# Performance work log

Measured on AMD Instinct MI355X. Metric: run time of the kernel, lower is better.

The kernel has to match this reference:

```python
import jax, jax.numpy as jnp
import numpy as np

STEP = 2  # neighbor window size (init arg `step`)


def _shift_sums(x, step):
    # sum over shifted-left (before) and shifted-right (after) neighbor states,
    # zero-padded at the boundaries, for shifts 1..step. x: [B, L, H]
    before = sum(jnp.pad(x[:, :-s, :], ((0, 0), (s, 0), (0, 0))) for s in range(1, step + 1))
    after = sum(jnp.pad(x[:, s:, :], ((0, 0), (0, s), (0, 0))) for s in range(1, step + 1))
    return before, after


def _slstm_forward(word_inputs, mask, num_layers, init_h, init_c, Wx, Wh, Wi, Wd, b, gWx, gWh, gb):
    B, L, D = word_inputs.shape
    H = Wx.shape[-1]
    fm = mask.astype(word_inputs.dtype)          # [B, L]
    seq_mask = fm[:, :, None]                    # [B, L, 1]
    mask_score = (fm * 1e25 - 1e25)[:, :, None]  # -inf-like for padded positions

    emb = word_inputs * seq_mask                 # embedding_hidden_state_pre
    h = (init_h * 0.1 - 0.05) * seq_mask         # uniform(-0.05, 0.05) init
    c = (init_c * 0.1 - 0.05) * seq_mask
    dh = jnp.mean(h, axis=1)                     # dummy-node hidden [B, H]
    dc = jnp.mean(c, axis=1)                     # dummy-node cell   [B, H]

    for _ in range(num_layers):
        comb = jnp.mean(h, axis=1)               # combined word hidden [B, H]
        dh_rep = jnp.broadcast_to(dh[:, None, :], (B, L, H))
        dc_rep = jnp.broadcast_to(dc[:, None, :], (B, L, H))

        # --- dummy (sentence) node update ---
        g_d = jax.nn.sigmoid(dh @ gWx[0] + comb @ gWh[0] + gb[0])              # [B, H]
        g_o = jax.nn.sigmoid(dh @ gWx[1] + comb @ gWh[1] + gb[1])              # [B, H]
        g_f = jax.nn.sigmoid(dh_rep @ gWx[2] + h @ gWh[2] + gb[2])             # [B, L, H]
        scores = jnp.concatenate([g_f + mask_score, g_d[:, None, :]], axis=1)  # [B, L+1, H]
        scores = jax.nn.softmax(scores, axis=1)
        dummy_c = jnp.sum(scores[:, :L, :] * c, axis=1) + scores[:, L, :] * dc
        dummy_h = g_o * jnp.tanh(dummy_c)

        # --- word node updates ---
        hb, ha = _shift_sums(h, STEP)
        cb, ca = _shift_sums(c, STEP)
        cat_h = jnp.concatenate([hb, ha], axis=-1)  # [B, L, 2H]

        # 7 gates stacked: f1, f2, f3, f4, i, o, u -> pre: [7, B, L, H]
        pre = (jnp.einsum('blh,ghk->gblk', h, Wx)
               + jnp.einsum('blh,ghk->gblk', cat_h, Wh)
               + jnp.einsum('bld,gdk->gblk', emb, Wi)
               + jnp.einsum('blh,ghk->gblk', dh_rep, Wd)
               + b[:, None, None, :])
        sig = jax.nn.sigmoid(pre[:6])
        f1, f2, f3, f4, i_g, o_g = sig[0], sig[1], sig[2], sig[3], sig[4], sig[5]
        u = jnp.tanh(pre[6])

        # normalize the five forget/input gates via softmax across gates
        five = jax.nn.softmax(jnp.stack([f1, f2, f3, f4, i_g], axis=0), axis=0)
        c_new = five[0] * cb + five[1] * ca + five[2] * c + five[3] * dc_rep + five[4] * u
        h_new = o_g * jnp.tanh(c_new)

        h = h_new * seq_mask
        c = c_new * seq_mask
        dh, dc = dummy_h, dummy_c

    return h


def setup_inputs() -> dict:
    key = jax.random.key(0)
    ks = jax.random.split(key, 12)
    B, L, D, H, G = 32, 1024, 256, 256, 7
    s = 0.1  # stddev of param init in the torch module
    return {
        'word_inputs': jax.random.normal(ks[0], (B, L, D), jnp.float32),
        'mask': jnp.ones((B, L), jnp.int32),
        'num_layers': 3,
        'init_h': jax.random.uniform(ks[1], (B, L, H), jnp.float32),
        'init_c': jax.random.uniform(ks[2], (B, L, H), jnp.float32),
        'Wx': jax.random.normal(ks[3], (G, H, H), jnp.float32) * s,
        'Wh': jax.random.normal(ks[4], (G, 2 * H, H), jnp.float32) * s,
        'Wi': jax.random.normal(ks[5], (G, D, H), jnp.float32) * s,
        'Wd': jax.random.normal(ks[6], (G, H, H), jnp.float32) * s,
        'b': jax.random.normal(ks[7], (G, H), jnp.float32) * s,
        'gWx': jax.random.normal(ks[8], (3, H, H), jnp.float32) * s,
        'gWh': jax.random.normal(ks[9], (3, H, H), jnp.float32) * s,
        'gb': jax.random.normal(ks[10], (3, H), jnp.float32) * s,
    }


def reference(word_inputs, mask, num_layers, init_h, init_c, Wx, Wh, Wi, Wd, b, gWx, gWh, gb):
    return _slstm_forward(word_inputs, mask, num_layers, init_h, init_c, Wx, Wh, Wi, Wd, b, gWx, gWh, gb)
```

## Files before the change

kernel.cpp:

```cpp
#include <hip/hip_runtime.h>
#include <hip/hip_bf16.h>
#include <math.h>

#define BB 32
#define LL 1024
#define DD 256
#define HH 256
#define NG 7
#define HW (HH*HH)
#define WhS (2*HH*HH)

typedef short bf16x8 __attribute__((ext_vector_type(8)));
typedef float f32x4  __attribute__((ext_vector_type(4)));
typedef unsigned short u16;
typedef unsigned int u32;

__device__ __forceinline__ float sigm(float x){ return 1.0f/(1.0f + expf(-x)); }
__device__ __forceinline__ float fsig(float x){ return __fdividef(1.0f, 1.0f + __expf(-x)); }
__device__ __forceinline__ float ftanh(float x){ return 1.0f - __fdividef(2.0f, 1.0f + __expf(2.0f*x)); }
__device__ __forceinline__ u16 f2b(float f){
  u32 u = __float_as_uint(f);
  return (u16)((u + 0x7fffu + ((u>>16)&1u)) >> 16);
}
__device__ __forceinline__ float b2f(u16 b){ return __uint_as_float(((u32)b)<<16); }
__device__ __forceinline__ float4 ld4(const float* p){ return *reinterpret_cast<const float4*>(p); }

__device__ __forceinline__ u32 packf2(float lo, float hi){
  float2 s; s.x = lo; s.y = hi;
  __hip_bfloat162 r = __float22bfloat162_rn(s);
  return *reinterpret_cast<u32*>(&r);
}
__device__ __forceinline__ u32 bfadd2(u32 a, u32 b){
  float lo = __uint_as_float(a << 16)        + __uint_as_float(b << 16);
  float hi = __uint_as_float(a & 0xffff0000u) + __uint_as_float(b & 0xffff0000u);
  return packf2(lo, hi);
}

__device__ __forceinline__ void gload16(const void* g, void* l){
  __builtin_amdgcn_global_load_lds(
    (const __attribute__((address_space(1))) unsigned int*)g,
    (__attribute__((address_space(3))) unsigned int*)l, 16, 0, 0);
}
__device__ __forceinline__ f32x4 mfma16(bf16x8 a, bf16x8 b, f32x4 c){
  return __builtin_amdgcn_mfma_f32_16x16x32_bf16(a, b, c, 0, 0, 0);
}

__global__ __launch_bounds__(256) void k_init(const float* __restrict__ ih, const float* __restrict__ ic,
    const int* __restrict__ mask, u16* __restrict__ h, float* __restrict__ c){
  size_t n = (size_t)BB*LL*HH;
  for (size_t idx = (size_t)blockIdx.x*256 + threadIdx.x; idx < n; idx += (size_t)gridDim.x*256){
    float fm = (float)mask[idx>>8];
    h[idx] = f2b((ih[idx]*0.1f - 0.05f)*fm);
    c[idx] = (ic[idx]*0.1f - 0.05f)*fm;
  }
}

__global__ __launch_bounds__(256) void k_mean1(const u16* __restrict__ h, const float* __restrict__ c,
    float* __restrict__ pmh, float* __restrict__ pmc){
  int b = blockIdx.x, ch = blockIdx.y, k = threadIdx.x;
  const u16* hp = h + ((size_t)b*LL + ch*64)*HH + k;
  const float* cp = c + ((size_t)b*LL + ch*64)*HH + k;
  float sh = 0.f, sc = 0.f;
  for (int l = 0; l < 64; ++l){ sh += b2f(hp[(size_t)l*HH]); sc += cp[(size_t)l*HH]; }
  pmh[(size_t)(b*16+ch)*HH + k] = sh;
  pmc[(size_t)(b*16+ch)*HH + k] = sc;
}
__global__ __launch_bounds__(256) void k_mean2(const float* __restrict__ pmh, const float* __restrict__ pmc,
    float* __restrict__ comb, float* __restrict__ combc){
  int b = blockIdx.x, k = threadIdx.x;
  float sh = 0.f, sc = 0.f;
  for (int ch = 0; ch < 16; ++ch){
    sh += pmh[(size_t)(b*16+ch)*HH + k];
    sc += pmc[(size_t)(b*16+ch)*HH + k];
  }
  comb[b*HH+k]  = sh*(1.0f/LL);
  combc[b*HH+k] = sc*(1.0f/LL);
}

__global__ __launch_bounds__(256) void k_small(const float* __restrict__ dh, const float* __restrict__ comb,
    const float* __restrict__ gWx, const float* __restrict__ gWh, const float* __restrict__ gb,
    const float* __restrict__ Wd, const float* __restrict__ bias,
    float* __restrict__ g_d, float* __restrict__ g_o, float* __restrict__ gx2f, float* __restrict__ wd){
  __shared__ float dsh[HH], csh[HH];
  int b = blockIdx.x, g = blockIdx.y, k = threadIdx.x;
  dsh[k] = dh[b*HH+k]; csh[k] = comb[b*HH+k];
  __syncthreads();
  if (g < NG){
    float aw = bias[g*HH+k];
    const float* W = Wd + (size_t)g*HW + k;
    for (int j = 0; j < HH; ++j) aw += dsh[j]*W[(size_t)j*HH];
    wd[(size_t)(g*BB + b)*HH + k] = aw;
  } else {
    float ad = gb[0*HH+k], ao = gb[1*HH+k], ax = gb[2*HH+k];
    for (int j = 0; j < HH; ++j){
      float dv = dsh[j], cv = csh[j];
      ad += dv*gWx[j*HH+k]      + cv*gWh[j*HH+k];
      ao += dv*gWx[HW + j*HH+k] + cv*gWh[HW + j*HH+k];
      ax += dv*gWx[2*HW + j*HH+k];
    }
    g_d[b*HH+k] = sigm(ad);
    g_o[b*HH+k] = sigm(ao);
    gx2f[b*HH+k] = ax;
  }
}

__global__ __launch_bounds__(256) void k_wpack(const float* __restrict__ Wx, const float* __restrict__ Wh,
    const float* __restrict__ Wi, u16* __restrict__ Bp){
  int idx = blockIdx.x*256 + threadIdx.x;
  int img = idx / 14336, e = idx % 14336;
  int nt = img >> 5, ks = img & 31;
  int g = e >> 11, r = e & 2047;
  int n = r >> 5, kblk = (r>>3)&3, j = r&7;
  int K = ks*32 + kblk*8 + j;
  int N = nt*64 + n;
  int slice = K >> 8, kr = K & 255;
  float v;
  if (slice == 0)      v = Wx[(size_t)g*HW  + (size_t)kr*HH + N];
  else if (slice == 1) v = Wh[(size_t)g*WhS + (size_t)kr*HH + N];
  else if (slice == 2) v = Wh[(size_t)g*WhS + (size_t)(256+kr)*HH + N];
  else                 v = Wi[(size_t)g*HW  + (size_t)kr*HH + N];
  Bp[idx] = f2b(v);
}

__global__ __launch_bounds__(256) void k_gw2pack(const float* __restrict__ gWh, u16* __restrict__ Gp){
  int idx = blockIdx.x*256 + threadIdx.x;
  int img = idx >> 11, r = idx & 2047;
  int nt = img >> 3, ks = img & 7;
  int n = r >> 5, kblk = (r>>3)&3, j = r&7;
  int K = ks*32 + kblk*8 + j, N = nt*64 + n;
  Gp[idx] = f2b(gWh[2*HW + (size_t)K*HH + N]);
}

__global__ __launch_bounds__(256) void k_dummy2(const float* __restrict__ pnumP, const float* __restrict__ pdenP,
    const float* __restrict__ g_d, const float* __restrict__ g_o, const float* __restrict__ dc,
    float* __restrict__ dh_n, float* __restrict__ dc_n){
  int b = blockIdx.x, k = threadIdx.x;
  float num = 0.f, den = 0.f;
  for (int mt = 0; mt < 16; ++mt){
    num += pnumP[(size_t)(b*16+mt)*HH + k];
    den += pdenP[(size_t)(b*16+mt)*HH + k];
  }
  float ed = expf(g_d[b*HH+k]);
  float v = (num + ed*dc[b*HH+k])/(den + ed);
  dc_n[b*HH+k] = v;
  dh_n[b*HH+k] = g_o[b*HH+k]*tanhf(v);
}

__global__ __launch_bounds__(256, 2) void k_main(const u16* __restrict__ h,
    const float* __restrict__ c,
    const float* __restrict__ win, const int* __restrict__ mask,
    const u16* __restrict__ Bp, const u16* __restrict__ Gp,
    const float* __restrict__ wd, const float* __restrict__ dc,
    const float* __restrict__ gx2f,
    u16* __restrict__ hout, float* __restrict__ cout, float* __restrict__ hf32,
    float* __restrict__ pnumP, float* __restrict__ pdenP, int wf32, int wc){
  __shared__ __align__(16) unsigned char lsA[2][4096];

  int tid = threadIdx.x, lane = tid & 63, wid = tid >> 6;
  int flat = blockIdx.x;
  int xcd = flat & 7, q = flat >> 3;
  int nt  = xcd >> 1;
  int mt  = (xcd & 1)*256 + q;
  int m0 = mt << 6, b = m0 >> 10;
  int li = lane & 15, kg = lane >> 4;

  int rA = wid*16 + (lane>>2);
  int kbA = (lane&3) ^ ((lane>>3)&3);
  int mA = m0 + rA, lpA = mA & (LL-1);
  float fmA = (float)mask[mA];

  int off0 = li*64 + ((kg ^ ((li>>1)&3))<<4);

  const unsigned char* bbase = (const unsigned char*)Bp
      + (size_t)nt*32*28672 + (size_t)(wid*16+li)*64 + (size_t)kg*16;
  const unsigned char* gbase = (const unsigned char*)Gp
      + (size_t)nt*8*4096  + (size_t)(wid*16+li)*64 + (size_t)kg*16;

  f32x4 acc[NG][4];
  f32x4 acc8[4];
  #pragma unroll
  for (int g=0; g<NG; ++g)
    #pragma unroll
    for (int mf=0; mf<4; ++mf) acc[g][mf] = (f32x4)0.f;
  #pragma unroll
  for (int mf=0; mf<4; ++mf) acc8[mf] = (f32x4)0.f;

  gload16(h + (size_t)mA*HH + kbA*8, lsA[0] + wid*1024);
  __syncthreads();

  int cur = 0;
  for (int ks = 0; ks < 32; ++ks){
    int nxt = cur ^ 1;
    const unsigned char* bstep = bbase + (size_t)ks*28672;
    bf16x8 bg[NG];
    #pragma unroll
    for (int g = 0; g < NG; ++g) bg[g] = *(const bf16x8*)(bstep + g*4096);
    bf16x8 b8;
    if (ks < 8) b8 = *(const bf16x8*)(gbase + (size_t)ks*4096);

    bool pend = false; uint4 pv;
    if (ks < 31){
      int kn = ks + 1, s1 = kn >> 3, co = (kn & 7)*32 + kbA*8;
      if (s1 == 0){
        gload16(h + (size_t)mA*HH + co, lsA[nxt] + wid*1024);
      } else if (s1 < 3){
        pend = true;
        int d = (s1 == 1) ? -(int)HH : (int)HH;
        bool e1 = (s1 == 1) ? (lpA >= 1) : (lpA <= LL-2);
        bool e2 = (s1 == 1) ? (lpA >= 2) : (lpA <= LL-3);
        const u16* hp = h + (size_t)mA*HH + co;
        uint4 u1 = make_uint4(0,0,0,0), u2 = make_uint4(0,0,0,0);
        if (e1) u1 = *(const uint4*)(hp + d);
        if (e2) u2 = *(const uint4*)(hp + 2*d);
        pv.x = bfadd2(u1.x, u2.x); pv.y = bfadd2(u1.y, u2.y);
        pv.z = bfadd2(u1.z, u2.z); pv.w = bfadd2(u1.w, u2.w);
      } else {
        pend = true;
        float4 w0 = ld4(win + (size_t)mA*DD + co);
        float4 w1 = ld4(win + (size_t)mA*DD + co + 4);
        pv.x = packf2(w0.x*fmA, w0.y*fmA); pv.y = packf2(w0.z*fmA, w0.w*fmA);
        pv.z = packf2(w1.x*fmA, w1.y*fmA); pv.w = packf2(w1.z*fmA, w1.w*fmA);
      }
    }

    bf16x8 aa[4];
    #pragma unroll
    for (int mf=0; mf<4; ++mf)
      aa[mf] = *(const bf16x8*)(lsA[cur] + mf*1024 + off0);
    __builtin_amdgcn_s_setprio(1);
    #pragma unroll
    for (int g = 0; g < NG; ++g)
      #pragma unroll
      for (int mf=0; mf<4; ++mf) acc[g][mf] = mfma16(aa[mf], bg[g], acc[g][mf]);
    if (ks < 8){
      #pragma unroll
      for (int mf=0; mf<4; ++mf) acc8[mf] = mfma16(aa[mf], b8, acc8[mf]);
    }
    __builtin_amdgcn_s_setprio(0);

    if (ks < 31){
      if (pend) *(uint4*)(lsA[nxt] + wid*1024 + lane*16) = pv;
      __syncthreads();
      cur = nxt;
    }
  }

  int col = nt*64 + wid*16 + li;
  float wdv[NG];
  #pragma unroll
  for (int g=0; g<NG; ++g) wdv[g] = wd[(size_t)(g*BB+b)*HH + col];
  float dcv = dc[b*HH + col];
  float gx  = gx2f[b*HH + col];
  float num = 0.f, den = 0.f;

  #pragma unroll
  for (int mf=0; mf<4; ++mf)
  #pragma unroll
  for (int j=0; j<4; ++j){
    int m = m0 + mf*16 + kg*4 + j;
    int lp = m & (LL-1);
    float fm = (float)mask[m];
    const float* cp = c + (size_t)m*HH + col;
    float cc = cp[0];
    float cbv = 0.f, cav = 0.f;
    if (lp >= 1)    cbv += cp[-(int)HH];
    if (lp >= 2)    cbv += cp[-2*(int)HH];
    if (lp <= LL-2) cav += cp[HH];
    if (lp <= LL-3) cav += cp[2*HH];
    float s0 = fsig(acc[0][mf][j] + wdv[0]);
    float s1 = fsig(acc[1][mf][j] + wdv[1]);
    float s2 = fsig(acc[2][mf][j] + wdv[2]);
    float s3 = fsig(acc[3][mf][j] + wdv[3]);
    float s4 = fsig(acc[4][mf][j] + wdv[4]);
    float s5 = fsig(acc[5][mf][j] + wdv[5]);
    float u  = ftanh(acc[6][mf][j] + wdv[6]);
    float e0 = __expf(s0), e1 = __expf(s1), e2 = __expf(s2), e3 = __expf(s3), e4 = __expf(s4);
    float inv = __fdividef(1.0f, e0+e1+e2+e3+e4);
    float cn = (e0*cbv + e1*cav + e2*cc + e3*dcv + e4*u)*inv;
    float hn = s5*ftanh(cn);
    hout[(size_t)m*HH + col] = f2b(hn*fm);
    if (wc)   cout[(size_t)m*HH + col] = cn*fm;
    if (wf32) hf32[(size_t)m*HH + col] = hn*fm;
    float s8 = fsig(acc8[mf][j] + gx);
    float e8 = fm * __expf(s8);
    num += e8 * cc;
    den += e8;
  }
  num += __shfl_xor(num, 16); num += __shfl_xor(num, 32);
  den += __shfl_xor(den, 16); den += __shfl_xor(den, 32);
  if (kg == 0){
    pnumP[(size_t)(m0>>6)*HH + col] = num;
    pdenP[(size_t)(m0>>6)*HH + col] = den;
  }
}

extern "C" void kernel_launch(void* const* d_in, const int* in_sizes, int n_in,
                              void* d_out, int out_size, void* d_ws, size_t ws_size,
                              hipStream_t stream) {
  const float* win   = (const float*)d_in[0];
  const int*   mask  = (const int*)d_in[1];
  const float* ih    = (const float*)d_in[3];
  const float* ic    = (const float*)d_in[4];
  const float* Wx    = (const float*)d_in[5];
  const float* Wh    = (const float*)d_in[6];
  const float* Wi    = (const float*)d_in[7];
  const float* Wd    = (const float*)d_in[8];
  const float* bias  = (const float*)d_in[9];
  const float* gWx   = (const float*)d_in[10];
  const float* gWh   = (const float*)d_in[11];
  const float* gb    = (const float*)d_in[12];

  const size_t SZ = (size_t)BB*LL*HH;
  char* p = (char*)d_ws;
  auto alloc = [&](size_t bytes)->char*{ char* r = p; p += (bytes + 255) & ~(size_t)255; return r; };
  u16*   hA    = (u16*)  alloc(SZ*2);
  u16*   hB    = (u16*)  alloc(SZ*2);
  float* cA    = (float*)alloc(SZ*4);
  float* cB    = (float*)d_out;
  u16*   Bp    = (u16*)  alloc((size_t)1835008*2);
  u16*   Gp    = (u16*)  alloc((size_t)65536*2);
  float* comb  = (float*)alloc(BB*HH*4);
  float* combc = (float*)alloc(BB*HH*4);
  float* dh0   = (float*)alloc(BB*HH*4);
  float* dh1   = (float*)alloc(BB*HH*4);
  float* dc0   = (float*)alloc(BB*HH*4);
  float* dc1   = (float*)alloc(BB*HH*4);
  float* g_d   = (float*)alloc(BB*HH*4);
  float* g_o   = (float*)alloc(BB*HH*4);
  float* gx2f  = (float*)alloc(BB*HH*4);
  float* wd    = (float*)alloc((size_t)NG*BB*HH*4);
  float* pnumP = (float*)alloc((size_t)512*HH*4);
  float* pdenP = (float*)alloc((size_t)512*HH*4);
  float* pmh   = (float*)alloc((size_t)BB*16*HH*4);
  float* pmc   = (float*)alloc((size_t)BB*16*HH*4);
  float* dhb[2] = {dh0, dh1};
  float* dcb[2] = {dc0, dc1};

  k_wpack<<<7168, 256, 0, stream>>>(Wx, Wh, Wi, Bp);
  k_gw2pack<<<256, 256, 0, stream>>>(gWh, Gp);
  k_init<<<2048, 256, 0, stream>>>(ih, ic, mask, hA, cA);

  u16 *h_cur = hA, *h_nxt = hB;
  float *c_cur = cA, *c_nxt = cB;
  for (int layer = 0; layer < 3; ++layer){
    k_mean1<<<dim3(BB,16), 256, 0, stream>>>(h_cur, c_cur, pmh, pmc);
    k_mean2<<<BB, 256, 0, stream>>>(pmh, pmc, comb, combc);
    const float* dh_l = (layer == 0) ? comb  : dhb[(layer+1)&1];
    const float* dc_l = (layer == 0) ? combc : dcb[(layer+1)&1];
    k_small<<<dim3(BB,8), 256, 0, stream>>>(dh_l, comb, gWx, gWh, gb, Wd, bias, g_d, g_o, gx2f, wd);
    int last = (layer == 2);
    k_main<<<2048, 256, 0, stream>>>(h_cur, c_cur, win, mask, Bp, Gp, wd, dc_l, gx2f,
                                     h_nxt, c_nxt, (float*)d_out, pnumP, pdenP, last, !last);
    k_dummy2<<<BB, 256, 0, stream>>>(pnumP, pdenP, g_d, g_o, dc_l, dhb[layer&1], dcb[layer&1]);
    u16* th = h_cur; h_cur = h_nxt; h_nxt = th;
    float* tc = c_cur; c_cur = c_nxt; c_nxt = tc;
  }
}
```

Measured before the change: 736.9 us.

## Stage full h tile with halo in LDS and split shifted-sum GEMMs

The main kernel now loads the block's 64 h rows plus a 2-row halo (68 rows) into LDS once, using zero-buffer sources at sequence boundaries. The old path built neighbor sums in registers per k-step and double-buffered them through LDS; now each shifted neighbor row is read straight from the staged tile and fed to a separate MFMA. The masked bf16 embeddings are precomputed once by a new pack kernel, and their GEMM reads directly from global memory. This removes per-step syncs and the bf16 neighbor adds, but doubles MFMA work for the neighbor terms and raises LDS use to about 36KB.

```diff
diff --git a/kernel.cpp b/kernel.cpp
--- a/kernel.cpp
+++ b/kernel.cpp
@@ -24,18 +24,11 @@
 }
 __device__ __forceinline__ float b2f(u16 b){ return __uint_as_float(((u32)b)<<16); }
 __device__ __forceinline__ float4 ld4(const float* p){ return *reinterpret_cast<const float4*>(p); }
-
 __device__ __forceinline__ u32 packf2(float lo, float hi){
   float2 s; s.x = lo; s.y = hi;
   __hip_bfloat162 r = __float22bfloat162_rn(s);
   return *reinterpret_cast<u32*>(&r);
 }
-__device__ __forceinline__ u32 bfadd2(u32 a, u32 b){
-  float lo = __uint_as_float(a << 16)        + __uint_as_float(b << 16);
-  float hi = __uint_as_float(a & 0xffff0000u) + __uint_as_float(b & 0xffff0000u);
-  return packf2(lo, hi);
-}
-
 __device__ __forceinline__ void gload16(const void* g, void* l){
   __builtin_amdgcn_global_load_lds(
     (const __attribute__((address_space(1))) unsigned int*)g,
@@ -53,6 +46,23 @@
     h[idx] = f2b((ih[idx]*0.1f - 0.05f)*fm);
     c[idx] = (ic[idx]*0.1f - 0.05f)*fm;
   }
+}
+
+__global__ __launch_bounds__(64) void k_zero(u16* __restrict__ zbuf){
+  ((uint4*)zbuf)[threadIdx.x & 31] = make_uint4(0,0,0,0);
+}
+
+__global__ __launch_bounds__(256) void k_embpack(const float* __restrict__ win,
+    const int* __restrict__ mask, u16* __restrict__ embp){
+  int idx = blockIdx.x*256 + threadIdx.x;
+  int m = idx >> 5, c8 = (idx & 31) << 3;
+  float fm = (float)mask[m];
+  float4 w0 = ld4(win + (size_t)m*DD + c8);
+  float4 w1 = ld4(win + (size_t)m*DD + c8 + 4);
+  uint4 pv;
+  pv.x = packf2(w0.x*fm, w0.y*fm); pv.y = packf2(w0.z*fm, w0.w*fm);
+  pv.z = packf2(w1.x*fm, w1.y*fm); pv.w = packf2(w1.z*fm, w1.w*fm);
+  *(uint4*)(embp + (size_t)m*HH + c8) = pv;
 }
 
 __global__ __launch_bounds__(256) void k_mean1(const u16* __restrict__ h, const float* __restrict__ c,
@@ -147,29 +157,23 @@
 }
 
 __global__ __launch_bounds__(256, 2) void k_main(const u16* __restrict__ h,
-    const float* __restrict__ c,
-    const float* __restrict__ win, const int* __restrict__ mask,
+    const float* __restrict__ c, const u16* __restrict__ embp,
+    const int* __restrict__ mask,
     const u16* __restrict__ Bp, const u16* __restrict__ Gp,
+    const u16* __restrict__ zbuf,
     const float* __restrict__ wd, const float* __restrict__ dc,
     const float* __restrict__ gx2f,
     u16* __restrict__ hout, float* __restrict__ cout, float* __restrict__ hf32,
     float* __restrict__ pnumP, float* __restrict__ pdenP, int wf32, int wc){
-  __shared__ __align__(16) unsigned char lsA[2][4096];
+  __shared__ __align__(16) unsigned char img[72*512];
 
   int tid = threadIdx.x, lane = tid & 63, wid = tid >> 6;
   int flat = blockIdx.x;
   int xcd = flat & 7, q = flat >> 3;
   int nt  = xcd >> 1;
   int mt  = (xcd & 1)*256 + q;
-  int m0 = mt << 6, b = m0 >> 10;
+  int m0 = mt << 6, b = m0 >> 10, l0 = m0 & (LL-1);
   int li = lane & 15, kg = lane >> 4;
-
-  int rA = wid*16 + (lane>>2);
-  int kbA = (lane&3) ^ ((lane>>3)&3);
-  int mA = m0 + rA, lpA = mA & (LL-1);
-  float fmA = (float)mask[mA];
-
-  int off0 = li*64 + ((kg ^ ((li>>1)&3))<<4);
 
   const unsigned char* bbase = (const unsigned char*)Bp
       + (size_t)nt*32*28672 + (size_t)(wid*16+li)*64 + (size_t)kg*16;
@@ -185,65 +189,105 @@
   #pragma unroll
   for (int mf=0; mf<4; ++mf) acc8[mf] = (f32x4)0.f;
 
-  gload16(h + (size_t)mA*HH + kbA*8, lsA[0] + wid*1024);
+  {
+    int row0 = lane >> 5, slot = lane & 31;
+    #pragma unroll
+    for (int k = 0; k < 9; ++k){
+      int ci = wid + 4*k;
+      int row = 2*ci + row0;
+      int col8 = slot ^ (row & 7);
+      int l = l0 - 2 + row;
+      const u16* src = (l >= 0 && l < LL && row < 68)
+                     ? (h + ((size_t)b*LL + l)*HH + col8*8)
+                     : (zbuf + col8*8);
+      gload16(src, img + ci*1024);
+    }
+  }
+
+  #pragma unroll 1
+  for (int t = 0; t < 8; ++t){
+    const unsigned char* bstep = bbase + (size_t)(24+t)*28672;
+    bf16x8 ea[4];
+    #pragma unroll
+    for (int mf=0; mf<4; ++mf)
+      ea[mf] = *(const bf16x8*)(embp + (size_t)(m0+mf*16+li)*HH + t*32 + kg*8);
+    __builtin_amdgcn_s_setprio(1);
+    #pragma unroll
+    for (int g = 0; g < NG; ++g){
+      bf16x8 bg = *(const bf16x8*)(bstep + g*4096);
+      #pragma unroll
+      for (int mf=0; mf<4; ++mf) acc[g][mf] = mfma16(ea[mf], bg, acc[g][mf]);
+    }
+    __builtin_amdgcn_s_setprio(0);
+  }
+
   __syncthreads();
 
-  int cur = 0;
-  for (int ks = 0; ks < 32; ++ks){
-    int nxt = cur ^ 1;
-    const unsigned char* bstep = bbase + (size_t)ks*28672;
-    bf16x8 bg[NG];
-    #pragma unroll
-    for (int g = 0; g < NG; ++g) bg[g] = *(const bf16x8*)(bstep + g*4096);
-    bf16x8 b8;
-    if (ks < 8) b8 = *(const bf16x8*)(gbase + (size_t)ks*4096);
-
-    bool pend = false; uint4 pv;
-    if (ks < 31){
-      int kn = ks + 1, s1 = kn >> 3, co = (kn & 7)*32 + kbA*8;
-      if (s1 == 0){
-        gload16(h + (size_t)mA*HH + co, lsA[nxt] + wid*1024);
-      } else if (s1 < 3){
-        pend = true;
-        int d = (s1 == 1) ? -(int)HH : (int)HH;
-        bool e1 = (s1 == 1) ? (lpA >= 1) : (lpA <= LL-2);
-        bool e2 = (s1 == 1) ? (lpA >= 2) : (lpA <= LL-3);
-        const u16* hp = h + (size_t)mA*HH + co;
-        uint4 u1 = make_uint4(0,0,0,0), u2 = make_uint4(0,0,0,0);
-        if (e1) u1 = *(const uint4*)(hp + d);
-        if (e2) u2 = *(const uint4*)(hp + 2*d);
-        pv.x = bfadd2(u1.x, u2.x); pv.y = bfadd2(u1.y, u2.y);
-        pv.z = bfadd2(u1.z, u2.z); pv.w = bfadd2(u1.w, u2.w);
-      } else {
-        pend = true;
-        float4 w0 = ld4(win + (size_t)mA*DD + co);
-        float4 w1 = ld4(win + (size_t)mA*DD + co + 4);
-        pv.x = packf2(w0.x*fmA, w0.y*fmA); pv.y = packf2(w0.z*fmA, w0.w*fmA);
-        pv.z = packf2(w1.x*fmA, w1.y*fmA); pv.w = packf2(w1.z*fmA, w1.w*fmA);
+  #define IMG(r, t) (*(const bf16x8*)(img + (r)*512 + ((((t)*4 + kg) ^ ((r)&7))<<4)))
+
+  #pragma unroll 1
+  for (int t = 0; t < 8; ++t){
+    const unsigned char* bstep = bbase + (size_t)t*28672;
+    bf16x8 aa[4];
+    #pragma unroll
+    for (int mf=0; mf<4; ++mf) aa[mf] = IMG(mf*16 + li + 2, t);
+    bf16x8 b8 = *(const bf16x8*)(gbase + (size_t)t*4096);
+    __builtin_amdgcn_s_setprio(1);
+    #pragma unroll
+    for (int g = 0; g < NG; ++g){
+      bf16x8 bg = *(const bf16x8*)(bstep + g*4096);
+      #pragma unroll
+      for (int mf=0; mf<4; ++mf) acc[g][mf] = mfma16(aa[mf], bg, acc[g][mf]);
+    }
+    #pragma unroll
+    for (int mf=0; mf<4; ++mf) acc8[mf] = mfma16(aa[mf], b8, acc8[mf]);
+    __builtin_amdgcn_s_setprio(0);
+  }
+
+  #pragma unroll 1
+  for (int t = 0; t < 8; ++t){
+    const unsigned char* bstep = bbase + (size_t)(8+t)*28672;
+    bf16x8 a0[4], a1[4];
+    #pragma unroll
+    for (int mf=0; mf<4; ++mf){
+      a1[mf] = IMG(mf*16 + li + 1, t);
+      a0[mf] = IMG(mf*16 + li + 0, t);
+    }
+    __builtin_amdgcn_s_setprio(1);
+    #pragma unroll
+    for (int g = 0; g < NG; ++g){
+      bf16x8 bg = *(const bf16x8*)(bstep + g*4096);
+      #pragma unroll
+      for (int mf=0; mf<4; ++mf){
+        acc[g][mf] = mfma16(a1[mf], bg, acc[g][mf]);
+        acc[g][mf] = mfma16(a0[mf], bg, acc[g][mf]);
       }
     }
-
-    bf16x8 aa[4];
-    #pragma unroll
-    for (int mf=0; mf<4; ++mf)
-      aa[mf] = *(const bf16x8*)(lsA[cur] + mf*1024 + off0);
+    __builtin_amdgcn_s_setprio(0);
+  }
+
+  #pragma unroll 1
+  for (int t = 0; t < 8; ++t){
+    const unsigned char* bstep = bbase + (size_t)(16+t)*28672;
+    bf16x8 a0[4], a1[4];
+    #pragma unroll
+    for (int mf=0; mf<4; ++mf){
+      a1[mf] = IMG(mf*16 + li + 3, t);
+      a0[mf] = IMG(mf*16 + li + 4, t);
+    }
     __builtin_amdgcn_s_setprio(1);
     #pragma unroll
-    for (int g = 0; g < NG; ++g)
+    for (int g = 0; g < NG; ++g){
+      bf16x8 bg = *(const bf16x8*)(bstep + g*4096);
       #pragma unroll
-      for (int mf=0; mf<4; ++mf) acc[g][mf] = mfma16(aa[mf], bg[g], acc[g][mf]);
-    if (ks < 8){
-      #pragma unroll
-      for (int mf=0; mf<4; ++mf) acc8[mf] = mfma16(aa[mf], b8, acc8[mf]);
+      for (int mf=0; mf<4; ++mf){
+        acc[g][mf] = mfma16(a1[mf], bg, acc[g][mf]);
+        acc[g][mf] = mfma16(a0[mf], bg, acc[g][mf]);
+      }
     }
     __builtin_amdgcn_s_setprio(0);
-
-    if (ks < 31){
-      if (pend) *(uint4*)(lsA[nxt] + wid*1024 + lane*16) = pv;
-      __syncthreads();
-      cur = nxt;
-    }
-  }
+  }
+  #undef IMG
 
   int col = nt*64 + wid*16 + li;
   float wdv[NG];
@@ -317,8 +361,10 @@
   u16*   hB    = (u16*)  alloc(SZ*2);
   float* cA    = (float*)alloc(SZ*4);
   float* cB    = (float*)d_out;
+  u16*   embp  = (u16*)  alloc(SZ*2);
   u16*   Bp    = (u16*)  alloc((size_t)1835008*2);
   u16*   Gp    = (u16*)  alloc((size_t)65536*2);
+  u16*   zbuf  = (u16*)  alloc(512);
   float* comb  = (float*)alloc(BB*HH*4);
   float* combc = (float*)alloc(BB*HH*4);
   float* dh0   = (float*)alloc(BB*HH*4);
@@ -338,6 +384,8 @@
 
   k_wpack<<<7168, 256, 0, stream>>>(Wx, Wh, Wi, Bp);
   k_gw2pack<<<256, 256, 0, stream>>>(gWh, Gp);
+  k_zero<<<1, 64, 0, stream>>>(zbuf);
+  k_embpack<<<4096, 256, 0, stream>>>(win, mask, embp);
   k_init<<<2048, 256, 0, stream>>>(ih, ic, mask, hA, cA);
 
   u16 *h_cur = hA, *h_nxt = hB;
@@ -349,7 +397,7 @@
     const float* dc_l = (layer == 0) ? combc : dcb[(layer+1)&1];
     k_small<<<dim3(BB,8), 256, 0, stream>>>(dh_l, comb, gWx, gWh, gb, Wd, bias, g_d, g_o, gx2f, wd);
     int last = (layer == 2);
-    k_main<<<2048, 256, 0, stream>>>(h_cur, c_cur, win, mask, Bp, Gp, wd, dc_l, gx2f,
+    k_main<<<2048, 256, 0, stream>>>(h_cur, c_cur, embp, mask, Bp, Gp, zbuf, wd, dc_l, gx2f,
                                      h_nxt, c_nxt, (float*)d_out, pnumP, pdenP, last, !last);
     k_dummy2<<<BB, 256, 0, stream>>>(pnumP, pdenP, g_d, g_o, dc_l, dhb[layer&1], dcb[layer&1]);
     u16* th = h_cur; h_cur = h_nxt; h_nxt = th;
```

New measurement: 820.6 us. 1.11x slower.

## Triple-buffer A tiles in groups of four k-steps and prepack embeddings to bf16

Applied to the files above, without the earlier changes.

The main GEMM loop now stages A operands four k-steps at a time into a three-deep LDS ring. It synchronises once per group with a partial vmcnt wait instead of one __syncthreads per k-step. The word-input embedding is masked and converted to bf16 once in a new pre-pass kernel, so the main kernel loads it through direct global-to-LDS loads like h instead of converting fp32 every layer. This cuts barrier count and per-layer conversion work, but LDS use grows to 48KB per block, which may limit occupancy at two blocks per CU. The hand-written vmcnt counts must also stay correct.

```diff
diff --git a/kernel.cpp b/kernel.cpp
--- a/kernel.cpp
+++ b/kernel.cpp
@@ -24,7 +24,6 @@
 }
 __device__ __forceinline__ float b2f(u16 b){ return __uint_as_float(((u32)b)<<16); }
 __device__ __forceinline__ float4 ld4(const float* p){ return *reinterpret_cast<const float4*>(p); }
-
 __device__ __forceinline__ u32 packf2(float lo, float hi){
   float2 s; s.x = lo; s.y = hi;
   __hip_bfloat162 r = __float22bfloat162_rn(s);
@@ -53,6 +52,19 @@
     h[idx] = f2b((ih[idx]*0.1f - 0.05f)*fm);
     c[idx] = (ic[idx]*0.1f - 0.05f)*fm;
   }
+}
+
+__global__ __launch_bounds__(256) void k_embpack(const float* __restrict__ win,
+    const int* __restrict__ mask, u16* __restrict__ embp){
+  int idx = blockIdx.x*256 + threadIdx.x;
+  int m = idx >> 5, c8 = (idx & 31) << 3;
+  float fm = (float)mask[m];
+  float4 w0 = ld4(win + (size_t)m*DD + c8);
+  float4 w1 = ld4(win + (size_t)m*DD + c8 + 4);
+  uint4 pv;
+  pv.x = packf2(w0.x*fm, w0.y*fm); pv.y = packf2(w0.z*fm, w0.w*fm);
+  pv.z = packf2(w1.x*fm, w1.y*fm); pv.w = packf2(w1.z*fm, w1.w*fm);
+  *(uint4*)(embp + (size_t)m*HH + c8) = pv;
 }
 
 __global__ __launch_bounds__(256) void k_mean1(const u16* __restrict__ h, const float* __restrict__ c,
@@ -147,14 +159,14 @@
 }
 
 __global__ __launch_bounds__(256, 2) void k_main(const u16* __restrict__ h,
-    const float* __restrict__ c,
-    const float* __restrict__ win, const int* __restrict__ mask,
+    const float* __restrict__ c, const u16* __restrict__ embp,
+    const int* __restrict__ mask,
     const u16* __restrict__ Bp, const u16* __restrict__ Gp,
     const float* __restrict__ wd, const float* __restrict__ dc,
     const float* __restrict__ gx2f,
     u16* __restrict__ hout, float* __restrict__ cout, float* __restrict__ hf32,
     float* __restrict__ pnumP, float* __restrict__ pdenP, int wf32, int wc){
-  __shared__ __align__(16) unsigned char lsA[2][4096];
+  __shared__ __align__(16) unsigned char lsA[3][4][4096];
 
   int tid = threadIdx.x, lane = tid & 63, wid = tid >> 6;
   int flat = blockIdx.x;
@@ -164,10 +176,9 @@
   int m0 = mt << 6, b = m0 >> 10;
   int li = lane & 15, kg = lane >> 4;
 
-  int rA = wid*16 + (lane>>2);
+  int rA = wid*16 + (lane>>2); (void)rA;
   int kbA = (lane&3) ^ ((lane>>3)&3);
-  int mA = m0 + rA, lpA = mA & (LL-1);
-  float fmA = (float)mask[mA];
+  int mA = m0 + wid*16 + (lane>>2), lpA = mA & (LL-1);
 
   int off0 = li*64 + ((kg ^ ((li>>1)&3))<<4);
 
@@ -185,64 +196,65 @@
   #pragma unroll
   for (int mf=0; mf<4; ++mf) acc8[mf] = (f32x4)0.f;
 
-  gload16(h + (size_t)mA*HH + kbA*8, lsA[0] + wid*1024);
-  __syncthreads();
-
-  int cur = 0;
-  for (int ks = 0; ks < 32; ++ks){
-    int nxt = cur ^ 1;
-    const unsigned char* bstep = bbase + (size_t)ks*28672;
-    bf16x8 bg[NG];
-    #pragma unroll
-    for (int g = 0; g < NG; ++g) bg[g] = *(const bf16x8*)(bstep + g*4096);
-    bf16x8 b8;
-    if (ks < 8) b8 = *(const bf16x8*)(gbase + (size_t)ks*4096);
-
-    bool pend = false; uint4 pv;
-    if (ks < 31){
-      int kn = ks + 1, s1 = kn >> 3, co = (kn & 7)*32 + kbA*8;
-      if (s1 == 0){
-        gload16(h + (size_t)mA*HH + co, lsA[nxt] + wid*1024);
-      } else if (s1 < 3){
-        pend = true;
-        int d = (s1 == 1) ? -(int)HH : (int)HH;
-        bool e1 = (s1 == 1) ? (lpA >= 1) : (lpA <= LL-2);
-        bool e2 = (s1 == 1) ? (lpA >= 2) : (lpA <= LL-3);
+  auto stage = [&](int Gs, int dst){
+    int base = 4*Gs, s1 = base >> 3;
+    if (s1 == 0 || s1 == 3){
+      const u16* src = (s1 == 0) ? h : embp;
+      #pragma unroll
+      for (int j=0;j<4;++j)
+        gload16(src + (size_t)mA*HH + ((base+j)&7)*32 + kbA*8, lsA[dst][j] + wid*1024);
+    } else {
+      int d = (s1 == 1) ? -(int)HH : (int)HH;
+      bool e1 = (s1 == 1) ? (lpA >= 1) : (lpA <= LL-2);
+      bool e2 = (s1 == 1) ? (lpA >= 2) : (lpA <= LL-3);
+      #pragma unroll
+      for (int j=0;j<4;++j){
+        int co = ((base+j)&7)*32 + kbA*8;
         const u16* hp = h + (size_t)mA*HH + co;
-        uint4 u1 = make_uint4(0,0,0,0), u2 = make_uint4(0,0,0,0);
-        if (e1) u1 = *(const uint4*)(hp + d);
-        if (e2) u2 = *(const uint4*)(hp + 2*d);
-        pv.x = bfadd2(u1.x, u2.x); pv.y = bfadd2(u1.y, u2.y);
-        pv.z = bfadd2(u1.z, u2.z); pv.w = bfadd2(u1.w, u2.w);
-      } else {
-        pend = true;
-        float4 w0 = ld4(win + (size_t)mA*DD + co);
-        float4 w1 = ld4(win + (size_t)mA*DD + co + 4);
-        pv.x = packf2(w0.x*fmA, w0.y*fmA); pv.y = packf2(w0.z*fmA, w0.w*fmA);
-        pv.z = packf2(w1.x*fmA, w1.y*fmA); pv.w = packf2(w1.z*fmA, w1.w*fmA);
+        uint4 u1 = e1 ? *(const uint4*)(hp + d)   : make_uint4(0,0,0,0);
+        uint4 u2 = e2 ? *(const uint4*)(hp + 2*d) : make_uint4(0,0,0,0);
+        uint4 pv;
+        pv.x = bfadd2(u1.x,u2.x); pv.y = bfadd2(u1.y,u2.y);
+        pv.z = bfadd2(u1.z,u2.z); pv.w = bfadd2(u1.w,u2.w);
+        *(uint4*)(lsA[dst][j] + wid*1024 + lane*16) = pv;
       }
     }
-
-    bf16x8 aa[4];
+  };
+
+  stage(0, 0);
+  stage(1, 1);
+  asm volatile("s_waitcnt vmcnt(4)" ::: "memory");
+  __builtin_amdgcn_s_barrier();
+
+  #pragma unroll 1
+  for (int G = 0; G < 8; ++G){
+    if (G < 6) stage(G+2, (G+2)%3);
+    int setc = G % 3;
     #pragma unroll
-    for (int mf=0; mf<4; ++mf)
-      aa[mf] = *(const bf16x8*)(lsA[cur] + mf*1024 + off0);
-    __builtin_amdgcn_s_setprio(1);
-    #pragma unroll
-    for (int g = 0; g < NG; ++g)
-      #pragma unroll
-      for (int mf=0; mf<4; ++mf) acc[g][mf] = mfma16(aa[mf], bg[g], acc[g][mf]);
-    if (ks < 8){
-      #pragma unroll
-      for (int mf=0; mf<4; ++mf) acc8[mf] = mfma16(aa[mf], b8, acc8[mf]);
+    for (int j = 0; j < 4; ++j){
+      int ks = 4*G + j;
+      const unsigned char* bstep = bbase + (size_t)ks*28672;
+      bf16x8 bg[NG];
+      #pragma unroll
+      for (int g = 0; g < NG; ++g) bg[g] = *(const bf16x8*)(bstep + g*4096);
+      bf16x8 aa[4];
+      #pragma unroll
+      for (int mf=0; mf<4; ++mf)
+        aa[mf] = *(const bf16x8*)(lsA[setc][j] + mf*1024 + off0);
+      __builtin_amdgcn_s_setprio(1);
+      #pragma unroll
+      for (int g = 0; g < NG; ++g)
+        #pragma unroll
+        for (int mf=0; mf<4; ++mf) acc[g][mf] = mfma16(aa[mf], bg[g], acc[g][mf]);
+      if (ks < 8){
+        bf16x8 b8 = *(const bf16x8*)(gbase + (size_t)ks*4096);
+        #pragma unroll
+        for (int mf=0; mf<4; ++mf) acc8[mf] = mfma16(aa[mf], b8, acc8[mf]);
+      }
+      __builtin_amdgcn_s_setprio(0);
     }
-    __builtin_amdgcn_s_setprio(0);
-
-    if (ks < 31){
-      if (pend) *(uint4*)(lsA[nxt] + wid*1024 + lane*16) = pv;
-      __syncthreads();
-      cur = nxt;
-    }
+    asm volatile("s_waitcnt vmcnt(4)" ::: "memory");
+    __builtin_amdgcn_s_barrier();
   }
 
   int col = nt*64 + wid*16 + li;
@@ -317,6 +329,7 @@
   u16*   hB    = (u16*)  alloc(SZ*2);
   float* cA    = (float*)alloc(SZ*4);
   float* cB    = (float*)d_out;
+  u16*   embp  = (u16*)  alloc(SZ*2);
   u16*   Bp    = (u16*)  alloc((size_t)1835008*2);
   u16*   Gp    = (u16*)  alloc((size_t)65536*2);
   float* comb  = (float*)alloc(BB*HH*4);
@@ -338,6 +351,7 @@
 
   k_wpack<<<7168, 256, 0, stream>>>(Wx, Wh, Wi, Bp);
   k_gw2pack<<<256, 256, 0, stream>>>(gWh, Gp);
+  k_embpack<<<4096, 256, 0, stream>>>(win, mask, embp);
   k_init<<<2048, 256, 0, stream>>>(ih, ic, mask, hA, cA);
 
   u16 *h_cur = hA, *h_nxt = hB;
@@ -349,7 +363,7 @@
     const float* dc_l = (layer == 0) ? combc : dcb[(layer+1)&1];
     k_small<<<dim3(BB,8), 256, 0, stream>>>(dh_l, comb, gWx, gWh, gb, Wd, bias, g_d, g_o, gx2f, wd);
     int last = (layer == 2);
-    k_main<<<2048, 256, 0, stream>>>(h_cur, c_cur, win, mask, Bp, Gp, wd, dc_l, gx2f,
+    k_main<<<2048, 256, 0, stream>>>(h_cur, c_cur, embp, mask, Bp, Gp, wd, dc_l, gx2f,
                                      h_nxt, c_nxt, (float*)d_out, pnumP, pdenP, last, !last);
     k_dummy2<<<BB, 256, 0, stream>>>(pnumP, pdenP, g_d, g_o, dc_l, dhb[layer&1], dcb[layer&1]);
     u16* th = h_cur; h_cur = h_nxt; h_nxt = th;
```

Result: faster. 694.9 us (-5.7%).
